# Kernel optimization log

Measured on AMD Instinct MI355X. Metric: run time of the kernel, lower is better.

The kernel has to match this reference:

```python
import jax, jax.numpy as jnp
import numpy as np

N = 524288          # events per batch
NUM_NODES = 1_000_000
D = 64              # memory_dim


def gru_cell(x, h, W_ih, W_hh, b_ih, b_hh):
    # torch.nn.GRUCell math; gates ordered (r, z, n)
    gi = x @ W_ih.T + b_ih          # [N, 3D]
    gh = h @ W_hh.T + b_hh          # [N, 3D]
    i_r, i_z, i_n = jnp.split(gi, 3, axis=-1)
    h_r, h_z, h_n = jnp.split(gh, 3, axis=-1)
    r = jax.nn.sigmoid(i_r + h_r)
    z = jax.nn.sigmoid(i_z + h_z)
    n = jnp.tanh(i_n + r * h_n)
    return (1.0 - z) * n + z * h


def setup_inputs() -> dict:
    key = jax.random.key(0)
    ks = jax.random.split(key, 9)
    scale = 1.0 / np.sqrt(D).astype(np.float32)
    return {
        "node_ids": jax.random.randint(ks[0], (N,), 0, NUM_NODES, dtype=jnp.int64)
        if jax.config.jax_enable_x64 else jax.random.randint(ks[0], (N,), 0, NUM_NODES, dtype=jnp.int32),
        "node_embeddings": jax.random.normal(ks[1], (N, D), jnp.float32),
        "timestamps": jax.random.uniform(ks[2], (N,), jnp.float32) * 1000.0,
        "node_memory": jax.random.normal(ks[3], (NUM_NODES, D), jnp.float32) * 0.1,
        "last_update_time": jax.random.uniform(ks[4], (NUM_NODES,), jnp.float32) * 500.0,
        "W_time": jax.random.normal(ks[5], (1, D), jnp.float32) * 0.1,
        "b_time": jnp.zeros((D,), jnp.float32),
        "W_ih": jax.random.normal(ks[6], (3 * D, D), jnp.float32) * scale,
        "W_hh": jax.random.normal(ks[7], (3 * D, D), jnp.float32) * scale,
        "b_ih": jnp.zeros((3 * D,), jnp.float32),
        "b_hh": jnp.zeros((3 * D,), jnp.float32),
    }


def reference(node_ids, node_embeddings, timestamps, node_memory, last_update_time,
              W_time, b_time, W_ih, W_hh, b_ih, b_hh):
    # gather persistent state
    current_memory = node_memory[node_ids]                          # [N, D]
    time_deltas = timestamps - last_update_time[node_ids]           # [N]
    # nn.Linear(1, D): out = dt * W_time[0] + b_time
    time_encoding = time_deltas[:, None] * W_time[0] + b_time       # [N, D]
    updated_memory = gru_cell(node_embeddings + time_encoding, current_memory,
                              W_ih, W_hh, b_ih, b_hh)               # [N, D]
    # scatter write-back (detached in torch)
    new_node_memory = node_memory.at[node_ids].set(jax.lax.stop_gradient(updated_memory))
    new_last_update_time = last_update_time.at[node_ids].set(jax.lax.stop_gradient(timestamps))
    return updated_memory, new_node_memory, new_last_update_time
```

## Files before the change

kernel.cpp:

```cpp
#include <hip/hip_runtime.h>
#include <cstdint>
#include <cstddef>

#define DD 64

typedef float    f32x4  __attribute__((ext_vector_type(4)));
typedef _Float16 f16x8  __attribute__((ext_vector_type(8)));
typedef _Float16 f16x4  __attribute__((ext_vector_type(4)));

__device__ __forceinline__ float sigmoidf_(float x) {
    return 1.0f / (1.0f + __expf(-x));
}
__device__ __forceinline__ float tanh_fast(float x) {
    float ax = fabsf(x);
    float t = 1.0f - 2.0f / (1.0f + __expf(2.0f * ax));
    return copysignf(t, x);
}
__device__ __forceinline__ f32x4 MFMA(f32x4 c, f16x8 a, f16x8 b) {
    return __builtin_amdgcn_mfma_f32_16x16x32_f16(a, b, c, 0, 0, 0);
}

__global__ void k_init(int* __restrict__ winner, int num_nodes) {
    int i = blockIdx.x * blockDim.x + threadIdx.x;
    if (i < num_nodes) winner[i] = -1;
}
__global__ void k_vote(const int* __restrict__ ids, int* __restrict__ winner, int n) {
    int i = blockIdx.x * blockDim.x + threadIdx.x;
    if (i < n) atomicMax(&winner[ids[i]], i);
}

__global__ void k_prep(const float* __restrict__ Wih, const float* __restrict__ Whh,
                       _Float16* __restrict__ bhi, _Float16* __restrict__ blo)
{
    int f = blockIdx.x;
    int l = threadIdx.x;
    int g = f >> 2, s = f & 3;
    int c = g * 16 + (l & 15);
    int grp = c >> 6, d = c & 63;
    int kbase = s * 32 + (l >> 4) * 8;
    int row = (grp == 0) ? d : (grp == 1) ? 64 + d : 128 + d;

    f16x8 hv, lv;
    for (int j = 0; j < 8; ++j) {
        int k = kbase + j;
        float v;
        if (grp <= 1)      v = (k < 64) ? Wih[row * 64 + k] : Whh[row * 64 + (k - 64)];
        else if (grp == 2) v = (k < 64) ? Wih[row * 64 + k] : 0.0f;
        else               v = (k < 64) ? 0.0f : Whh[row * 64 + (k - 64)];
        _Float16 h = (_Float16)v;
        hv[j] = h;
        lv[j] = (_Float16)(v - (float)h);
    }
    size_t off = ((size_t)f * 64 + l);
    ((f16x8*)bhi)[off] = hv;
    ((f16x8*)blo)[off] = lv;
}

__global__ __launch_bounds__(256, 3) void k_gru(
    const int* __restrict__ ids,
    const float* __restrict__ emb,
    const float* __restrict__ ts,
    const float* __restrict__ mem,
    const float* __restrict__ lut,
    const float* __restrict__ Wt,
    const float* __restrict__ bt,
    const float* __restrict__ bih,
    const float* __restrict__ bhh,
    const _Float16* __restrict__ bhi,
    const _Float16* __restrict__ blo,
    const int* __restrict__ winner,
    float* __restrict__ out0,
    float* __restrict__ out1,
    int n)
{
    __shared__ _Float16 xhh[64][136];
    __shared__ _Float16 xhl[64][72];
    __shared__ int sid[64];
    __shared__ int swin[64];

    const int w    = threadIdx.x >> 6;
    const int l    = threadIdx.x & 63;
    const int col  = l & 15;
    const int rowg = l >> 4;
    const int d    = w * 16 + col;

    const long base = (long)blockIdx.x * 64;
    const bool full = (base + 64 <= (long)n);

    const int  e16 = w * 16 + col;
    const long evA = base + e16;
    int idA = 0, winA = 0; float dtA = 0.f;
    if (full || evA < n) {
        idA  = ids[evA];
        dtA  = ts[evA] - lut[idA];
        winA = (winner[idA] == (int)evA) ? 1 : 0;
    }
    if (l < 16) { sid[e16] = idA; swin[e16] = winA; }

    f32x4 xv0, xv1, xv2, xv3, hv0, hv1, hv2, hv3;
    float dt0, dt1, dt2, dt3;
    {
        int   i0 = __shfl(idA, 0 * 4 + rowg), i1 = __shfl(idA, 1 * 4 + rowg);
        int   i2 = __shfl(idA, 2 * 4 + rowg), i3 = __shfl(idA, 3 * 4 + rowg);
        dt0 = __shfl(dtA, 0 * 4 + rowg); dt1 = __shfl(dtA, 1 * 4 + rowg);
        dt2 = __shfl(dtA, 2 * 4 + rowg); dt3 = __shfl(dtA, 3 * 4 + rowg);
        const f32x4* emb4 = (const f32x4*)emb;
        const f32x4* mem4 = (const f32x4*)mem;
        const size_t e0 = (size_t)(base + w * 16 + 0 * 4 + rowg) * 16 + col;
        const size_t e1 = (size_t)(base + w * 16 + 1 * 4 + rowg) * 16 + col;
        const size_t e2 = (size_t)(base + w * 16 + 2 * 4 + rowg) * 16 + col;
        const size_t e3 = (size_t)(base + w * 16 + 3 * 4 + rowg) * 16 + col;
        if (full) {
            xv0 = __builtin_nontemporal_load(&emb4[e0]);
            xv1 = __builtin_nontemporal_load(&emb4[e1]);
            xv2 = __builtin_nontemporal_load(&emb4[e2]);
            xv3 = __builtin_nontemporal_load(&emb4[e3]);
            hv0 = mem4[(size_t)i0 * 16 + col];
            hv1 = mem4[(size_t)i1 * 16 + col];
            hv2 = mem4[(size_t)i2 * 16 + col];
            hv3 = mem4[(size_t)i3 * 16 + col];
        } else {
            f32x4 z = {0.f, 0.f, 0.f, 0.f};
            xv0 = xv1 = xv2 = xv3 = hv0 = hv1 = hv2 = hv3 = z;
            if (base + w * 16 + 0 * 4 + rowg < n) { xv0 = emb4[e0]; hv0 = mem4[(size_t)i0 * 16 + col]; }
            if (base + w * 16 + 1 * 4 + rowg < n) { xv1 = emb4[e1]; hv1 = mem4[(size_t)i1 * 16 + col]; }
            if (base + w * 16 + 2 * 4 + rowg < n) { xv2 = emb4[e2]; hv2 = mem4[(size_t)i2 * 16 + col]; }
            if (base + w * 16 + 3 * 4 + rowg < n) { xv3 = emb4[e3]; hv3 = mem4[(size_t)i3 * 16 + col]; }
        }
    }

    const f32x4 wt4 = ((const f32x4*)Wt)[col];
    const f32x4 bt4 = ((const f32x4*)bt)[col];
    {
        #define CONV_WRITE(XV, HV, DT, IT)                                           \
        {                                                                            \
            int r = w * 16 + (IT) * 4 + rowg;                                        \
            f32x4 x = XV;                                                            \
            x.x = fmaf(DT, wt4.x, x.x + bt4.x);                                      \
            x.y = fmaf(DT, wt4.y, x.y + bt4.y);                                      \
            x.z = fmaf(DT, wt4.z, x.z + bt4.z);                                      \
            x.w = fmaf(DT, wt4.w, x.w + bt4.w);                                      \
            f16x4 xh, xl, hh;                                                        \
            _Float16 a;                                                              \
            a = (_Float16)x.x; xh[0] = a; xl[0] = (_Float16)(x.x - (float)a);        \
            a = (_Float16)x.y; xh[1] = a; xl[1] = (_Float16)(x.y - (float)a);        \
            a = (_Float16)x.z; xh[2] = a; xl[2] = (_Float16)(x.z - (float)a);        \
            a = (_Float16)x.w; xh[3] = a; xl[3] = (_Float16)(x.w - (float)a);        \
            hh[0] = (_Float16)(HV).x; hh[1] = (_Float16)(HV).y;                      \
            hh[2] = (_Float16)(HV).z; hh[3] = (_Float16)(HV).w;                      \
            *(f16x4*)&xhh[r][col * 4]      = xh;                                     \
            *(f16x4*)&xhl[r][col * 4]      = xl;                                     \
            *(f16x4*)&xhh[r][64 + col * 4] = hh;                                     \
        }
        CONV_WRITE(xv0, hv0, dt0, 0)
        CONV_WRITE(xv1, hv1, dt1, 1)
        CONV_WRITE(xv2, hv2, dt2, 2)
        CONV_WRITE(xv3, hv3, dt3, 3)
        #undef CONV_WRITE
    }

    const f16x8* H = (const f16x8*)bhi;
    const f16x8* L = (const f16x8*)blo;
    f16x8 BRh0 = H[(size_t)(w * 4 + 0) * 64 + l];
    f16x8 BRh1 = H[(size_t)(w * 4 + 1) * 64 + l];
    f16x8 BRh2 = H[(size_t)(w * 4 + 2) * 64 + l];
    f16x8 BRh3 = H[(size_t)(w * 4 + 3) * 64 + l];
    f16x8 BRl0 = L[(size_t)(w * 4 + 0) * 64 + l];
    f16x8 BRl1 = L[(size_t)(w * 4 + 1) * 64 + l];
    f16x8 BZh0 = H[(size_t)((4 + w) * 4 + 0) * 64 + l];
    f16x8 BZh1 = H[(size_t)((4 + w) * 4 + 1) * 64 + l];
    f16x8 BZh2 = H[(size_t)((4 + w) * 4 + 2) * 64 + l];
    f16x8 BZh3 = H[(size_t)((4 + w) * 4 + 3) * 64 + l];
    f16x8 BZl0 = L[(size_t)((4 + w) * 4 + 0) * 64 + l];
    f16x8 BZl1 = L[(size_t)((4 + w) * 4 + 1) * 64 + l];
    f16x8 BIh0 = H[(size_t)((8 + w) * 4 + 0) * 64 + l];
    f16x8 BIh1 = H[(size_t)((8 + w) * 4 + 1) * 64 + l];
    f16x8 BIl0 = L[(size_t)((8 + w) * 4 + 0) * 64 + l];
    f16x8 BIl1 = L[(size_t)((8 + w) * 4 + 1) * 64 + l];
    f16x8 BHh0 = H[(size_t)((12 + w) * 4 + 2) * 64 + l];
    f16x8 BHh1 = H[(size_t)((12 + w) * 4 + 3) * 64 + l];

    const float bR  = bih[d] + bhh[d];
    const float bZ  = bih[64 + d] + bhh[64 + d];
    const float bIN = bih[128 + d];
    const float bHN = bhh[128 + d];

    __syncthreads();

    #pragma unroll
    for (int mt = 0; mt < 4; ++mt) {
        const int arow = mt * 16 + col;
        const int k0   = rowg * 8;
        f16x8 Ah0 = *(const f16x8*)&xhh[arow][0 * 32 + k0];
        f16x8 Ah1 = *(const f16x8*)&xhh[arow][1 * 32 + k0];
        f16x8 Ah2 = *(const f16x8*)&xhh[arow][2 * 32 + k0];
        f16x8 Ah3 = *(const f16x8*)&xhh[arow][3 * 32 + k0];
        f16x8 Al0 = *(const f16x8*)&xhl[arow][0 * 32 + k0];
        f16x8 Al1 = *(const f16x8*)&xhl[arow][1 * 32 + k0];

        f32x4 aR = {0,0,0,0}, aZ = {0,0,0,0}, aI = {0,0,0,0}, aH = {0,0,0,0};
        __builtin_amdgcn_s_setprio(1);
        aR = MFMA(aR, Ah0, BRh0); aR = MFMA(aR, Ah0, BRl0); aR = MFMA(aR, Al0, BRh0);
        aR = MFMA(aR, Ah1, BRh1); aR = MFMA(aR, Ah1, BRl1); aR = MFMA(aR, Al1, BRh1);
        aR = MFMA(aR, Ah2, BRh2); aR = MFMA(aR, Ah3, BRh3);
        aZ = MFMA(aZ, Ah0, BZh0); aZ = MFMA(aZ, Ah0, BZl0); aZ = MFMA(aZ, Al0, BZh0);
        aZ = MFMA(aZ, Ah1, BZh1); aZ = MFMA(aZ, Ah1, BZl1); aZ = MFMA(aZ, Al1, BZh1);
        aZ = MFMA(aZ, Ah2, BZh2); aZ = MFMA(aZ, Ah3, BZh3);
        aI = MFMA(aI, Ah0, BIh0); aI = MFMA(aI, Ah0, BIl0); aI = MFMA(aI, Al0, BIh0);
        aI = MFMA(aI, Ah1, BIh1); aI = MFMA(aI, Ah1, BIl1); aI = MFMA(aI, Al1, BIh1);
        aH = MFMA(aH, Ah2, BHh0); aH = MFMA(aH, Ah3, BHh1);
        __builtin_amdgcn_s_setprio(0);

        #pragma unroll
        for (int r = 0; r < 4; ++r) {
            int  eloc = mt * 16 + rowg * 4 + r;
            long ev   = base + eloc;
            if (full || ev < n) {
                float rr = sigmoidf_(aR[r] + bR);
                float zz = sigmoidf_(aZ[r] + bZ);
                float nn = tanh_fast(aI[r] + bIN + rr * (aH[r] + bHN));
                float hv = (float)xhh[eloc][64 + d];
                float o  = (1.f - zz) * nn + zz * hv;
                __builtin_nontemporal_store(o, &out0[(size_t)ev * 64 + d]);
                if (swin[eloc])
                    __builtin_nontemporal_store(o, &out1[(size_t)sid[eloc] * 64 + d]);
            }
        }
    }
}

__global__ void k_tail(float* out2,
                       const f32x4* __restrict__ mem4,
                       f32x4* __restrict__ out14,
                       const float* __restrict__ ts,
                       const float* __restrict__ lut,
                       int num_nodes)
{
    int idx = blockIdx.x * blockDim.x + threadIdx.x;
    if (idx >= num_nodes * 16) return;
    int nidx = idx >> 4;
    int c    = idx & 15;
    int wv = reinterpret_cast<const int*>(out2)[nidx];
    if (wv < 0) {
        f32x4 v = __builtin_nontemporal_load(&mem4[idx]);
        __builtin_nontemporal_store(v, &out14[idx]);
    }
    if (c == 0) out2[nidx] = (wv >= 0) ? ts[wv] : lut[nidx];
}

extern "C" void kernel_launch(void* const* d_in, const int* in_sizes, int n_in,
                              void* d_out, int out_size, void* d_ws, size_t ws_size,
                              hipStream_t stream) {
    const int*   ids = (const int*)  d_in[0];
    const float* emb = (const float*)d_in[1];
    const float* ts  = (const float*)d_in[2];
    const float* mem = (const float*)d_in[3];
    const float* lut = (const float*)d_in[4];
    const float* Wt  = (const float*)d_in[5];
    const float* bt  = (const float*)d_in[6];
    const float* Wih = (const float*)d_in[7];
    const float* Whh = (const float*)d_in[8];
    const float* bih = (const float*)d_in[9];
    const float* bhh = (const float*)d_in[10];

    const int N         = in_sizes[0];
    const int NUM_NODES = in_sizes[4];

    float* out0 = (float*)d_out;
    float* out1 = out0 + (size_t)N * DD;
    float* out2 = out1 + (size_t)NUM_NODES * DD;
    int*   winner = (int*)out2;

    _Float16* bfragH = (_Float16*)d_ws;
    _Float16* bfragL = bfragH + 64 * 64 * 8;

    k_prep<<<64, 64, 0, stream>>>(Wih, Whh, bfragH, bfragL);
    k_init<<<(NUM_NODES + 255) / 256, 256, 0, stream>>>(winner, NUM_NODES);
    k_vote<<<(N + 255) / 256, 256, 0, stream>>>(ids, winner, N);

    int nchunks = (N + 63) / 64;
    k_gru<<<nchunks, 256, 0, stream>>>(ids, emb, ts, mem, lut, Wt, bt, bih, bhh,
                                       bfragH, bfragL, winner, out0, out1, N);

    long vec = (long)NUM_NODES * 16;
    k_tail<<<(int)((vec + 255) / 256), 256, 0, stream>>>(
        out2, (const f32x4*)mem, (f32x4*)out1, ts, lut, NUM_NODES);
}
```

Before: 233.0 us.

## Fuse tail copy into GRU kernel via interleaved block roles; merge prep and init

The node-memory copy and last-update-time write (the tail) now run inside the main GRU kernel. Two of every three blocks do tail work and the third does a GRU chunk, so the bandwidth-bound copy overlaps with the MFMA compute instead of running as a separate kernel afterwards. The weight-prep and winner-init kernels are merged into one launch. The winner array moves from aliasing out2 into the workspace, so tail and GRU blocks can run at the same time without a read/write hazard. The cost is block-role divergence, shared-memory allocation even in tail blocks, and a dependence on the workspace being large enough.

```diff
diff --git a/kernel.cpp b/kernel.cpp
--- a/kernel.cpp
+++ b/kernel.cpp
@@ -20,43 +20,45 @@
     return __builtin_amdgcn_mfma_f32_16x16x32_f16(a, b, c, 0, 0, 0);
 }
 
-__global__ void k_init(int* __restrict__ winner, int num_nodes) {
-    int i = blockIdx.x * blockDim.x + threadIdx.x;
-    if (i < num_nodes) winner[i] = -1;
-}
+__global__ void k_prep_init(const float* __restrict__ Wih, const float* __restrict__ Whh,
+                            _Float16* __restrict__ bhi, _Float16* __restrict__ blo,
+                            int* __restrict__ winner, int num_nodes)
+{
+    if (blockIdx.x < 16) {
+        int f = blockIdx.x * 4 + (threadIdx.x >> 6);
+        int l = threadIdx.x & 63;
+        int g = f >> 2, s = f & 3;
+        int c = g * 16 + (l & 15);
+        int grp = c >> 6, dd = c & 63;
+        int kbase = s * 32 + (l >> 4) * 8;
+        int row = (grp == 0) ? dd : (grp == 1) ? 64 + dd : 128 + dd;
+
+        f16x8 hv, lv;
+        for (int j = 0; j < 8; ++j) {
+            int k = kbase + j;
+            float v;
+            if (grp <= 1)      v = (k < 64) ? Wih[row * 64 + k] : Whh[row * 64 + (k - 64)];
+            else if (grp == 2) v = (k < 64) ? Wih[row * 64 + k] : 0.0f;
+            else               v = (k < 64) ? 0.0f : Whh[row * 64 + (k - 64)];
+            _Float16 h = (_Float16)v;
+            hv[j] = h;
+            lv[j] = (_Float16)(v - (float)h);
+        }
+        size_t off = ((size_t)f * 64 + l);
+        ((f16x8*)bhi)[off] = hv;
+        ((f16x8*)blo)[off] = lv;
+    } else {
+        int i = (int)(blockIdx.x - 16) * 256 + threadIdx.x;
+        if (i < num_nodes) winner[i] = -1;
+    }
+}
+
 __global__ void k_vote(const int* __restrict__ ids, int* __restrict__ winner, int n) {
     int i = blockIdx.x * blockDim.x + threadIdx.x;
     if (i < n) atomicMax(&winner[ids[i]], i);
 }
 
-__global__ void k_prep(const float* __restrict__ Wih, const float* __restrict__ Whh,
-                       _Float16* __restrict__ bhi, _Float16* __restrict__ blo)
-{
-    int f = blockIdx.x;
-    int l = threadIdx.x;
-    int g = f >> 2, s = f & 3;
-    int c = g * 16 + (l & 15);
-    int grp = c >> 6, d = c & 63;
-    int kbase = s * 32 + (l >> 4) * 8;
-    int row = (grp == 0) ? d : (grp == 1) ? 64 + d : 128 + d;
-
-    f16x8 hv, lv;
-    for (int j = 0; j < 8; ++j) {
-        int k = kbase + j;
-        float v;
-        if (grp <= 1)      v = (k < 64) ? Wih[row * 64 + k] : Whh[row * 64 + (k - 64)];
-        else if (grp == 2) v = (k < 64) ? Wih[row * 64 + k] : 0.0f;
-        else               v = (k < 64) ? 0.0f : Whh[row * 64 + (k - 64)];
-        _Float16 h = (_Float16)v;
-        hv[j] = h;
-        lv[j] = (_Float16)(v - (float)h);
-    }
-    size_t off = ((size_t)f * 64 + l);
-    ((f16x8*)bhi)[off] = hv;
-    ((f16x8*)blo)[off] = lv;
-}
-
-__global__ __launch_bounds__(256, 3) void k_gru(
+__global__ __launch_bounds__(256, 3) void k_main(
     const int* __restrict__ ids,
     const float* __restrict__ emb,
     const float* __restrict__ ts,
@@ -71,20 +73,45 @@
     const int* __restrict__ winner,
     float* __restrict__ out0,
     float* __restrict__ out1,
-    int n)
+    float* __restrict__ out2,
+    int n, int num_nodes)
 {
     __shared__ _Float16 xhh[64][136];
     __shared__ _Float16 xhl[64][72];
     __shared__ int sid[64];
     __shared__ int swin[64];
 
+    const unsigned bt3 = blockIdx.x % 3;
+    if (bt3 != 0) {
+        int tail_idx = 2 * (int)(blockIdx.x / 3) + ((int)bt3 - 1);
+        int node = tail_idx * 64 + ((int)threadIdx.x >> 2);
+        if (node >= num_nodes) return;
+        int q  = (int)threadIdx.x & 3;
+        int wv = winner[node];
+        if (wv < 0) {
+            const f32x4* mem4  = (const f32x4*)mem;
+            f32x4*       out14 = (f32x4*)out1;
+            size_t o = (size_t)node * 16 + q * 4;
+            f32x4 v0 = __builtin_nontemporal_load(&mem4[o + 0]);
+            f32x4 v1 = __builtin_nontemporal_load(&mem4[o + 1]);
+            f32x4 v2 = __builtin_nontemporal_load(&mem4[o + 2]);
+            f32x4 v3 = __builtin_nontemporal_load(&mem4[o + 3]);
+            __builtin_nontemporal_store(v0, &out14[o + 0]);
+            __builtin_nontemporal_store(v1, &out14[o + 1]);
+            __builtin_nontemporal_store(v2, &out14[o + 2]);
+            __builtin_nontemporal_store(v3, &out14[o + 3]);
+        }
+        if (q == 0) out2[node] = (wv >= 0) ? ts[wv] : lut[node];
+        return;
+    }
+
     const int w    = threadIdx.x >> 6;
     const int l    = threadIdx.x & 63;
     const int col  = l & 15;
     const int rowg = l >> 4;
     const int d    = w * 16 + col;
 
-    const long base = (long)blockIdx.x * 64;
+    const long base = (long)(blockIdx.x / 3) * 64;
     const bool full = (base + 64 <= (long)n);
 
     const int  e16 = w * 16 + col;
@@ -229,25 +256,6 @@
     }
 }
 
-__global__ void k_tail(float* out2,
-                       const f32x4* __restrict__ mem4,
-                       f32x4* __restrict__ out14,
-                       const float* __restrict__ ts,
-                       const float* __restrict__ lut,
-                       int num_nodes)
-{
-    int idx = blockIdx.x * blockDim.x + threadIdx.x;
-    if (idx >= num_nodes * 16) return;
-    int nidx = idx >> 4;
-    int c    = idx & 15;
-    int wv = reinterpret_cast<const int*>(out2)[nidx];
-    if (wv < 0) {
-        f32x4 v = __builtin_nontemporal_load(&mem4[idx]);
-        __builtin_nontemporal_store(v, &out14[idx]);
-    }
-    if (c == 0) out2[nidx] = (wv >= 0) ? ts[wv] : lut[nidx];
-}
-
 extern "C" void kernel_launch(void* const* d_in, const int* in_sizes, int n_in,
                               void* d_out, int out_size, void* d_ws, size_t ws_size,
                               hipStream_t stream) {
@@ -269,20 +277,19 @@
     float* out0 = (float*)d_out;
     float* out1 = out0 + (size_t)N * DD;
     float* out2 = out1 + (size_t)NUM_NODES * DD;
-    int*   winner = (int*)out2;
 
     _Float16* bfragH = (_Float16*)d_ws;
     _Float16* bfragL = bfragH + 64 * 64 * 8;
-
-    k_prep<<<64, 64, 0, stream>>>(Wih, Whh, bfragH, bfragL);
-    k_init<<<(NUM_NODES + 255) / 256, 256, 0, stream>>>(winner, NUM_NODES);
+    int*      winner = (int*)((char*)d_ws + 128 * 1024);
+
+    int initBlocks = (NUM_NODES + 255) / 256;
+    k_prep_init<<<16 + initBlocks, 256, 0, stream>>>(Wih, Whh, bfragH, bfragL,
+                                                     winner, NUM_NODES);
     k_vote<<<(N + 255) / 256, 256, 0, stream>>>(ids, winner, N);
 
-    int nchunks = (N + 63) / 64;
-    k_gru<<<nchunks, 256, 0, stream>>>(ids, emb, ts, mem, lut, Wt, bt, bih, bhh,
-                                       bfragH, bfragL, winner, out0, out1, N);
-
-    long vec = (long)NUM_NODES * 16;
-    k_tail<<<(int)((vec + 255) / 256), 256, 0, stream>>>(
-        out2, (const f32x4*)mem, (f32x4*)out1, ts, lut, NUM_NODES);
-}
+    int gruBlocks  = (N + 63) / 64;
+    int totalBlocks = gruBlocks * 3;
+    k_main<<<totalBlocks, 256, 0, stream>>>(ids, emb, ts, mem, lut, Wt, bt, bih, bhh,
+                                            bfragH, bfragL, winner, out0, out1, out2,
+                                            N, NUM_NODES);
+}
```

After: 290.0 us. 24.5% more time.
